# Kernel optimization log

Hardware: AMD Instinct MI355X
Metric: run time of the kernel (lower is better)

## Reference

```python
import jax, jax.numpy as jnp
import numpy as np

OBS = 256      # observation_space_size == state_vector_len
SV = 2047      # STATE_VECTORS = WMG_MAX_OBS
D = 256        # tfm_vec_size = 8 heads * 32 head_size
H = 8
HD = 32
L = 2          # TFM_NUM_LAYERS
FF = 1024      # TFM_HIDDEN_SIZE
ACH = 512      # AC_HIDDEN_LAYER_SIZE
A = 16         # action_space_size


def setup_inputs() -> dict:
    key = jax.random.key(0)
    ks = jax.random.split(key, 24)
    r = lambda k, s: (jax.random.normal(k, s, jnp.float32) * 0.02)
    inp = {
        "observation": jax.random.normal(ks[0], (OBS,), jnp.float32),
        "old_vectors": jax.random.normal(ks[1], (SV, OBS), jnp.float32),
        "W_core": r(ks[2], (OBS, D)), "b_core": jnp.zeros((D,), jnp.float32),
        # memo embedding takes cat(state_vec, age_onehot) of size OBS+SV
        "W_memo": r(ks[3], (OBS + SV, D)), "b_memo": jnp.zeros((D,), jnp.float32),
        "Wq": r(ks[4], (L, D, D)), "bq": jnp.zeros((L, D), jnp.float32),
        "Wk": r(ks[5], (L, D, D)), "bk": jnp.zeros((L, D), jnp.float32),
        "Wv": r(ks[6], (L, D, D)), "bv": jnp.zeros((L, D), jnp.float32),
        "Wo": r(ks[7], (L, D, D)), "bo": jnp.zeros((L, D), jnp.float32),
        "ln1_g": jnp.ones((L, D), jnp.float32), "ln1_b": jnp.zeros((L, D), jnp.float32),
        "ln2_g": jnp.ones((L, D), jnp.float32), "ln2_b": jnp.zeros((L, D), jnp.float32),
        "W_ff1": r(ks[8], (L, D, FF)), "b_ff1": jnp.zeros((L, FF), jnp.float32),
        "W_ff2": r(ks[9], (L, FF, D)), "b_ff2": jnp.zeros((L, D), jnp.float32),
        "aW1": r(ks[10], (D, ACH)), "ab1": jnp.zeros((ACH,), jnp.float32),
        "aW2": r(ks[11], (ACH, ACH)), "ab2": jnp.zeros((ACH,), jnp.float32),
        "aWo": r(ks[12], (ACH, A)), "abo": jnp.zeros((A,), jnp.float32),
        "cW1": r(ks[13], (D, ACH)), "cb1": jnp.zeros((ACH,), jnp.float32),
        "cW2": r(ks[14], (ACH, ACH)), "cb2": jnp.zeros((ACH,), jnp.float32),
        "cWo": r(ks[15], (ACH, 1)), "cbo": jnp.zeros((1,), jnp.float32),
    }
    return inp


def _ln(x, g, b, eps=1e-5):
    m = jnp.mean(x, axis=-1, keepdims=True)
    v = jnp.mean(jnp.square(x - m), axis=-1, keepdims=True)
    return (x - m) * jax.lax.rsqrt(v + eps) * g + b


def reference(observation, old_vectors, W_core, b_core, W_memo, b_memo,
              Wq, bq, Wk, bk, Wv, bv, Wo, bo,
              ln1_g, ln1_b, ln2_g, ln2_b, W_ff1, b_ff1, W_ff2, b_ff2,
              aW1, ab1, aW2, ab2, aWo, abo, cW1, cb1, cW2, cb2, cWo, cbo):
    # core embedding [D]
    emb0 = observation @ W_core + b_core
    # fused memo + age-onehot embedding: cat(vec_i, e_i) @ W_memo == vec_i @ W_memo[:OBS] + W_memo[OBS+i]
    memo_emb = old_vectors @ W_memo[:OBS] + W_memo[OBS:] + b_memo  # [SV, D]
    x = jnp.concatenate([emb0[None, :], memo_emb], axis=0)[None]   # [1, 1+SV, D]
    S = 1 + SV
    scale = 1.0 / np.sqrt(HD).astype(np.float32)
    for l in range(L):
        q = (x @ Wq[l] + bq[l]).reshape(1, S, H, HD)
        k = (x @ Wk[l] + bk[l]).reshape(1, S, H, HD)
        v = (x @ Wv[l] + bv[l]).reshape(1, S, H, HD)
        scores = jnp.einsum('bqhd,bkhd->bhqk', q, k) * scale       # [1,H,S,S]
        probs = jax.nn.softmax(scores, axis=-1)
        ctx = jnp.einsum('bhqk,bkhd->bqhd', probs, v).reshape(1, S, D)
        x = _ln(x + ctx @ Wo[l] + bo[l], ln1_g[l], ln1_b[l])
        h = jax.nn.gelu(x @ W_ff1[l] + b_ff1[l])
        x = _ln(x + h @ W_ff2[l] + b_ff2[l], ln2_g[l], ln2_b[l])
    t = x[:, 0, :]                                                 # [1, D]
    ha = jnp.tanh(jnp.tanh(t @ aW1 + ab1) @ aW2 + ab2)
    policy = ha @ aWo + abo                                        # [1, A] logits
    hc = jnp.tanh(jnp.tanh(t @ cW1 + cb1) @ cW2 + cb2)
    value_est = hc @ cWo + cbo                                     # [1, 1]
    # WMG_MAX_MEMOS == 0 path: new state vector is tanh(observation)
    new_vector = jnp.tanh(observation)                             # [OBS]
    return value_est, policy, new_vector
```

## Files before the change

kernel.cpp:

```cpp
#include <hip/hip_runtime.h>
#include <stdint.h>

typedef __attribute__((ext_vector_type(8))) short bf16x8;
typedef __attribute__((ext_vector_type(4))) float f32x4;

constexpr int kSEQ = 2048;
constexpr int kD   = 256;
constexpr int kHD  = 32;
constexpr int kFF  = 1024;
constexpr int kACH = 512;
constexpr int kA   = 16;

__device__ __forceinline__ unsigned short f2b(float f) {
  union { float f; unsigned int u; } v; v.f = f;
  unsigned int r = v.u + 0x7FFFu + ((v.u >> 16) & 1u);
  return (unsigned short)(r >> 16);
}

struct ConvTable {
  const float* src[14];
  int K[14];
  int N[14];
  int dst[14];
  int tstart[15];
};

union SharedU {
  struct { unsigned short lt[64][72]; } cv;
  struct { unsigned short Al[64][40]; unsigned short Bl[64][40]; } g64;
  struct { unsigned short Kl[64][40]; unsigned short Vt[32][72];
           unsigned short Pl[4][16][72]; } at;
  struct { unsigned short As[16][264]; float2 red[4][16]; } lg;
  struct { float tl[512]; float red[4][64]; } hd;
  struct { float ha[512]; float hc[512]; float vred[4]; } h3;
};

struct MegaParams {
  ConvTable tab;
  const float *obs, *oldv, *Wcore, *bcore, *bmemo, *Wmemo2;
  const float *bq, *bk, *bv, *bo, *ln1g, *ln1b, *ln2g, *ln2b, *bff1, *bff2;
  const float *aW1, *ab1, *aW2, *ab2, *aWo, *abo;
  const float *cW1, *cb1, *cW2, *cb2, *cWo, *cbo;
  float* xf; unsigned short* xb;
  unsigned short *qb, *kb, *vb, *hb, *wT;
  float *pacc, *pml, *h1, *h2, *out;
  int oMemo, oQKV[2], oWoT[2], oFF1[2], oFF2[2];
  int convJobs, nsplit, tpb;
};

__device__ void ph_conv(const MegaParams& p, SharedU& sh) {
  const int tid = threadIdx.x;
  for (int job = blockIdx.x; job <= p.convJobs; job += gridDim.x) {
    __syncthreads();
    if (job == p.convJobs) {
      float a = p.bcore[tid];
      #pragma unroll 8
      for (int k = 0; k < 256; k++) a += p.obs[k] * p.Wcore[k * kD + tid];
      p.xf[tid] = a;
      p.xb[tid] = f2b(a);
      continue;
    }
    int m = 0;
    while (job >= p.tab.tstart[m + 1]) m++;
    const int tloc = job - p.tab.tstart[m];
    const int N = p.tab.N[m], K = p.tab.K[m];
    const int ntile = N >> 6;
    const int k0 = (tloc / ntile) * 64, n0 = (tloc % ntile) * 64;
    const float* src = p.tab.src[m];
    {
      const int r = tid >> 2, c16 = (tid & 3) * 16;
      const float* sp = src + (size_t)(k0 + r) * N + n0 + c16;
      #pragma unroll
      for (int j = 0; j < 16; j++) sh.cv.lt[r][c16 + j] = f2b(sp[j]);
    }
    __syncthreads();
    {
      const int n = tid >> 2, kc = (tid & 3) * 16;
      unsigned short* dp = p.wT + p.tab.dst[m] + (size_t)(n0 + n) * K + k0 + kc;
      unsigned short g[16];
      #pragma unroll
      for (int j = 0; j < 16; j++) g[j] = sh.cv.lt[kc + j][n];
      *(bf16x8*)dp = *(bf16x8*)&g[0];
      *(bf16x8*)(dp + 8) = *(bf16x8*)&g[8];
    }
  }
}

template <int EPI, bool AF32>
__device__ __forceinline__ void gemm64_job(
    SharedU& sh, int m0, int n0, const void* Ap, int lda, int M, int K,
    const unsigned short* BT, const float* p0, const float* p1,
    const float* p2, void* o0, void* o1, void* o2) {
  const int tid = threadIdx.x;
  const int w = tid >> 6, l = tid & 63, lg = l >> 4, lr = l & 15;
  const int sr = tid >> 2, sk = (tid & 3) * 8;
  f32x4 acc[4];
  #pragma unroll
  for (int c = 0; c < 4; c++)
    #pragma unroll
    for (int i = 0; i < 4; i++) acc[c][i] = 0.f;

  auto loadA = [&](int k0) -> bf16x8 {
    bf16x8 av;
    if (m0 + sr < M) {
      if constexpr (AF32) {
        const float* ap = (const float*)Ap + (size_t)(m0 + sr) * lda + k0 + sk;
        #pragma unroll
        for (int j = 0; j < 8; j++) av[j] = (short)f2b(ap[j]);
      } else {
        av = *(const bf16x8*)((const unsigned short*)Ap +
                              (size_t)(m0 + sr) * lda + k0 + sk);
      }
    } else {
      #pragma unroll
      for (int j = 0; j < 8; j++) av[j] = 0;
    }
    return av;
  };

  bf16x8 av = loadA(0);
  bf16x8 bv = *(const bf16x8*)(BT + (size_t)(n0 + sr) * K + sk);

  for (int k0 = 0; k0 < K; k0 += 32) {
    __syncthreads();
    *(bf16x8*)&sh.g64.Al[sr][sk] = av;
    *(bf16x8*)&sh.g64.Bl[sr][sk] = bv;
    __syncthreads();
    if (k0 + 32 < K) {
      av = loadA(k0 + 32);
      bv = *(const bf16x8*)(BT + (size_t)(n0 + sr) * K + k0 + 32 + sk);
    }
    bf16x8 af = *(bf16x8*)&sh.g64.Al[w * 16 + lr][8 * lg];
    #pragma unroll
    for (int c = 0; c < 4; c++) {
      bf16x8 bf = *(bf16x8*)&sh.g64.Bl[c * 16 + lr][8 * lg];
      acc[c] = __builtin_amdgcn_mfma_f32_16x16x32_bf16(af, bf, acc[c], 0, 0, 0);
    }
  }

  #pragma unroll
  for (int c = 0; c < 4; c++) {
    #pragma unroll
    for (int i = 0; i < 4; i++) {
      const int gr = m0 + w * 16 + 4 * lg + i;
      const int gc = n0 + c * 16 + lr;
      if (gr >= M) continue;
      float v = acc[c][i];
      if constexpr (EPI == 0) {
        v += p0[gc] + p1[(size_t)gr * kD + gc];
        ((float*)o0)[(size_t)(gr + 1) * kD + gc] = v;
        ((unsigned short*)o1)[(size_t)(gr + 1) * kD + gc] = f2b(v);
      } else if constexpr (EPI == 1) {
        const int t = gc >> 8, cc = gc & 255;
        const float* bp = (t == 0) ? p0 : (t == 1 ? p1 : p2);
        unsigned short* op = (t == 0) ? (unsigned short*)o0
                              : (t == 1 ? (unsigned short*)o1
                                        : (unsigned short*)o2);
        v += bp[cc];
        if (t == 0) v *= 0.17677669529663687f;
        op[(size_t)gr * kD + cc] = f2b(v);
      } else {
        v += p0[gc];
        const float g =
            0.5f * v *
            (1.0f + tanhf(0.7978845608028654f * (v + 0.044715f * v * v * v)));
        ((unsigned short*)o0)[(size_t)gr * kFF + gc] = f2b(g);
      }
    }
  }
}

template <int EPI, bool AF32>
__device__ void ph_gemm(SharedU& sh, const void* Ap, int lda, int M, int K,
                        const unsigned short* BT, int Mtiles, int Ntiles,
                        const float* p0, const float* p1, const float* p2,
                        void* o0, void* o1, void* o2) {
  const int njobs = Mtiles * Ntiles;
  for (int job = blockIdx.x; job < njobs; job += gridDim.x) {
    const int m0 = (job % Mtiles) * 64, n0 = (job / Mtiles) * 64;
    gemm64_job<EPI, AF32>(sh, m0, n0, Ap, lda, M, K, BT, p0, p1, p2, o0, o1, o2);
  }
}

__device__ void attn_job(SharedU& sh, int qb_, int h, int s, int tpb,
                         const unsigned short* q, const unsigned short* k,
                         const unsigned short* v, float* pacc, float* pml) {
  const int tid = threadIdx.x;
  const int w = tid >> 6, l = tid & 63, lg = l >> 4, lr = l & 15;
  const int q0 = qb_ * 64;
  const int hoff = h * kHD;
  const int sr = tid >> 2, sk = (tid & 3) * 8;
  const int t0 = s * tpb;

  const bf16x8 qf =
      *(const bf16x8*)(q + (size_t)(q0 + w * 16 + lr) * kD + hoff + 8 * lg);

  float m_[4], l_[4];
  f32x4 acc[2];
  #pragma unroll
  for (int i = 0; i < 4; i++) { m_[i] = -1e30f; l_[i] = 0.f; }
  #pragma unroll
  for (int dt = 0; dt < 2; dt++)
    #pragma unroll
    for (int i = 0; i < 4; i++) acc[dt][i] = 0.f;

  bf16x8 kreg = *(const bf16x8*)(k + (size_t)(t0 * 64 + sr) * kD + hoff + sk);
  bf16x8 vreg = *(const bf16x8*)(v + (size_t)(t0 * 64 + sr) * kD + hoff + sk);

  for (int t = 0; t < tpb; t++) {
    __syncthreads();
    *(bf16x8*)&sh.at.Kl[sr][sk] = kreg;
    #pragma unroll
    for (int j = 0; j < 8; j++) sh.at.Vt[sk + j][sr] = (unsigned short)vreg[j];
    __syncthreads();
    if (t + 1 < tpb) {
      const size_t nx = (size_t)((t0 + t + 1) * 64 + sr) * kD + hoff + sk;
      kreg = *(const bf16x8*)(k + nx);
      vreg = *(const bf16x8*)(v + nx);
    }
    f32x4 sc[4];
    #pragma unroll
    for (int c = 0; c < 4; c++) {
      f32x4 z;
      #pragma unroll
      for (int i = 0; i < 4; i++) z[i] = 0.f;
      bf16x8 kf = *(bf16x8*)&sh.at.Kl[c * 16 + lr][8 * lg];
      sc[c] = __builtin_amdgcn_mfma_f32_16x16x32_bf16(qf, kf, z, 0, 0, 0);
    }
    float tm[4];
    #pragma unroll
    for (int i = 0; i < 4; i++)
      tm[i] = fmaxf(fmaxf(sc[0][i], sc[1][i]), fmaxf(sc[2][i], sc[3][i]));
    #pragma unroll
    for (int mm = 1; mm <= 8; mm <<= 1)
      #pragma unroll
      for (int i = 0; i < 4; i++) tm[i] = fmaxf(tm[i], __shfl_xor(tm[i], mm));
    float pv[4][4], rs[4], corr[4];
    #pragma unroll
    for (int i = 0; i < 4; i++) {
      const float nm = fmaxf(m_[i], tm[i]);
      corr[i] = __expf(m_[i] - nm);
      m_[i] = nm;
      rs[i] = 0.f;
    }
    #pragma unroll
    for (int c = 0; c < 4; c++)
      #pragma unroll
      for (int i = 0; i < 4; i++) {
        pv[c][i] = __expf(sc[c][i] - m_[i]);
        rs[i] += pv[c][i];
      }
    #pragma unroll
    for (int mm = 1; mm <= 8; mm <<= 1)
      #pragma unroll
      for (int i = 0; i < 4; i++) rs[i] += __shfl_xor(rs[i], mm);
    #pragma unroll
    for (int i = 0; i < 4; i++) {
      l_[i] = l_[i] * corr[i] + rs[i];
      acc[0][i] *= corr[i];
      acc[1][i] *= corr[i];
    }
    #pragma unroll
    for (int c = 0; c < 4; c++)
      #pragma unroll
      for (int i = 0; i < 4; i++)
        sh.at.Pl[w][4 * lg + i][c * 16 + lr] = f2b(pv[c][i]);
    __syncthreads();
    #pragma unroll
    for (int k2 = 0; k2 < 2; k2++) {
      bf16x8 pf = *(bf16x8*)&sh.at.Pl[w][lr][k2 * 32 + 8 * lg];
      #pragma unroll
      for (int dt = 0; dt < 2; dt++) {
        bf16x8 vf = *(bf16x8*)&sh.at.Vt[dt * 16 + lr][k2 * 32 + 8 * lg];
        acc[dt] = __builtin_amdgcn_mfma_f32_16x16x32_bf16(pf, vf, acc[dt], 0, 0, 0);
      }
    }
  }

  const int pb = s * 8 + h;
  float* pa = pacc + (size_t)pb * kSEQ * kHD;
  float* pm = pml + (size_t)pb * kSEQ * 2;
  #pragma unroll
  for (int dt = 0; dt < 2; dt++)
    #pragma unroll
    for (int i = 0; i < 4; i++) {
      const int gr = q0 + w * 16 + 4 * lg + i;
      pa[(size_t)gr * kHD + dt * 16 + lr] = acc[dt][i];
    }
  if (lr == 0) {
    #pragma unroll
    for (int i = 0; i < 4; i++) {
      const int gr = q0 + w * 16 + 4 * lg + i;
      float2 ml; ml.x = m_[i]; ml.y = l_[i];
      *(float2*)&pm[(size_t)gr * 2] = ml;
    }
  }
}

__device__ void ph_attn(const MegaParams& p, SharedU& sh) {
  const int njobs = 256 * p.nsplit;
  for (int job = blockIdx.x; job < njobs; job += gridDim.x) {
    const int qb_ = job & 31, h = (job >> 5) & 7, s = job >> 8;
    attn_job(sh, qb_, h, s, p.tpb, p.qb, p.kb, p.vb, p.pacc, p.pml);
  }
}

__device__ __forceinline__ void ln_write(SharedU& sh, float vloc[4][4], int r0,
                                         const float* gam, const float* bet,
                                         float* xf, unsigned short* xb) {
  const int tid = threadIdx.x;
  const int w = tid >> 6, l = tid & 63, lg = l >> 4, lr = l & 15;
  float ps[4], ps2[4];
  #pragma unroll
  for (int i = 0; i < 4; i++) {
    ps[i] = 0.f; ps2[i] = 0.f;
    #pragma unroll
    for (int c = 0; c < 4; c++) {
      ps[i] += vloc[c][i];
      ps2[i] += vloc[c][i] * vloc[c][i];
    }
  }
  #pragma unroll
  for (int mm = 1; mm <= 8; mm <<= 1)
    #pragma unroll
    for (int i = 0; i < 4; i++) {
      ps[i] += __shfl_xor(ps[i], mm);
      ps2[i] += __shfl_xor(ps2[i], mm);
    }
  if (lr == 0) {
    #pragma unroll
    for (int i = 0; i < 4; i++) {
      float2 t; t.x = ps[i]; t.y = ps2[i];
      sh.lg.red[w][4 * lg + i] = t;
    }
  }
  __syncthreads();
  #pragma unroll
  for (int i = 0; i < 4; i++) {
    const int ri = 4 * lg + i;
    float sx = 0.f, sx2 = 0.f;
    #pragma unroll
    for (int ww = 0; ww < 4; ww++) {
      float2 t = sh.lg.red[ww][ri];
      sx += t.x; sx2 += t.y;
    }
    const float mean = sx * (1.0f / 256.0f);
    const float var = sx2 * (1.0f / 256.0f) - mean * mean;
    const float rstd = rsqrtf(var + 1e-5f);
    const int gr = r0 + ri;
    #pragma unroll
    for (int c = 0; c < 4; c++) {
      const int col = w * 64 + c * 16 + lr;
      const float y = (vloc[c][i] - mean) * rstd * gam[col] + bet[col];
      xf[(size_t)gr * kD + col] = y;
      xb[(size_t)gr * kD + col] = f2b(y);
    }
  }
}

__device__ void ph_woln(const MegaParams& p, SharedU& sh, int lyr) {
  const unsigned short* BT = p.wT + p.oWoT[lyr];
  const float* bias = p.bo + lyr * kD;
  const float* gam = p.ln1g + lyr * kD;
  const float* bet = p.ln1b + lyr * kD;
  const int tid = threadIdx.x;
  const int w = tid >> 6, l = tid & 63, lg = l >> 4, lr = l & 15;
  for (int job = blockIdx.x; job < 128; job += gridDim.x) {
    const int r0 = job * 16;
    __syncthreads();
    {
      const int row = r0 + (tid >> 4);
      const int kc = (tid & 15) * 16;
      const int h_ = kc >> 5;
      float mx = -1e30f;
      float mlm[4], mll[4];
      for (int s2 = 0; s2 < p.nsplit; s2++) {
        const float2 t =
            *(const float2*)&p.pml[((size_t)(s2 * 8 + h_) * kSEQ + row) * 2];
        mlm[s2] = t.x; mll[s2] = t.y;
        mx = fmaxf(mx, t.x);
      }
      float L = 0.f, e[4];
      for (int s2 = 0; s2 < p.nsplit; s2++) {
        e[s2] = __expf(mlm[s2] - mx);
        L += mll[s2] * e[s2];
      }
      const float inv = 1.0f / L;
      const int d0 = kc & 31;
      float o[16];
      #pragma unroll
      for (int j = 0; j < 16; j++) o[j] = 0.f;
      for (int s2 = 0; s2 < p.nsplit; s2++) {
        const float* pa =
            p.pacc + ((size_t)(s2 * 8 + h_) * kSEQ + row) * kHD + d0;
        const float es = e[s2];
        #pragma unroll
        for (int j = 0; j < 16; j++) o[j] += pa[j] * es;
      }
      unsigned short* dst = &sh.lg.As[tid >> 4][kc];
      #pragma unroll
      for (int j = 0; j < 16; j++) dst[j] = f2b(o[j] * inv);
    }
    __syncthreads();
    f32x4 acc[4];
    #pragma unroll
    for (int c = 0; c < 4; c++)
      #pragma unroll
      for (int i = 0; i < 4; i++) acc[c][i] = 0.f;
    #pragma unroll 2
    for (int k0 = 0; k0 < 256; k0 += 32) {
      bf16x8 af = *(bf16x8*)&sh.lg.As[lr][k0 + 8 * lg];
      #pragma unroll
      for (int c = 0; c < 4; c++) {
        bf16x8 bf = *(const bf16x8*)(BT + (size_t)(w * 64 + c * 16 + lr) * 256 +
                                     k0 + 8 * lg);
        acc[c] = __builtin_amdgcn_mfma_f32_16x16x32_bf16(af, bf, acc[c], 0, 0, 0);
      }
    }
    float vloc[4][4];
    #pragma unroll
    for (int c = 0; c < 4; c++)
      #pragma unroll
      for (int i = 0; i < 4; i++) {
        const int col = w * 64 + c * 16 + lr;
        const int gr = r0 + 4 * lg + i;
        vloc[c][i] = acc[c][i] + bias[col] + p.xf[(size_t)gr * kD + col];
      }
    ln_write(sh, vloc, r0, gam, bet, p.xf, p.xb);
  }
}

__device__ void ph_ff2ln(const MegaParams& p, SharedU& sh, int lyr) {
  const unsigned short* BT = p.wT + p.oFF2[lyr];
  const float* bias = p.bff2 + lyr * kD;
  const float* gam = p.ln2g + lyr * kD;
  const float* bet = p.ln2b + lyr * kD;
  const int tid = threadIdx.x;
  const int w = tid >> 6, l = tid & 63, lg = l >> 4, lr = l & 15;
  for (int job = blockIdx.x; job < 128; job += gridDim.x) {
    const int r0 = job * 16;
    f32x4 acc[4];
    #pragma unroll
    for (int c = 0; c < 4; c++)
      #pragma unroll
      for (int i = 0; i < 4; i++) acc[c][i] = 0.f;
    const int srow = tid >> 4, skc = (tid & 15) * 16;
    const unsigned short* src = p.hb + (size_t)(r0 + srow) * kFF + skc;
    bf16x8 a0 = *(const bf16x8*)src;
    bf16x8 a1 = *(const bf16x8*)(src + 8);
    for (int kc = 0; kc < 1024; kc += 256) {
      __syncthreads();
      *(bf16x8*)&sh.lg.As[srow][skc] = a0;
      *(bf16x8*)&sh.lg.As[srow][skc + 8] = a1;
      __syncthreads();
      if (kc + 256 < 1024) {
        a0 = *(const bf16x8*)(src + kc + 256);
        a1 = *(const bf16x8*)(src + kc + 256 + 8);
      }
      #pragma unroll 2
      for (int k0 = 0; k0 < 256; k0 += 32) {
        bf16x8 af = *(bf16x8*)&sh.lg.As[lr][k0 + 8 * lg];
        #pragma unroll
        for (int c = 0; c < 4; c++) {
          bf16x8 bf = *(const bf16x8*)(
              BT + (size_t)(w * 64 + c * 16 + lr) * 1024 + kc + k0 + 8 * lg);
          acc[c] = __builtin_amdgcn_mfma_f32_16x16x32_bf16(af, bf, acc[c], 0, 0, 0);
        }
      }
    }
    float vloc[4][4];
    #pragma unroll
    for (int c = 0; c < 4; c++)
      #pragma unroll
      for (int i = 0; i < 4; i++) {
        const int col = w * 64 + c * 16 + lr;
        const int gr = r0 + 4 * lg + i;
        vloc[c][i] = acc[c][i] + bias[col] + p.xf[(size_t)gr * kD + col];
      }
    ln_write(sh, vloc, r0, gam, bet, p.xf, p.xb);
  }
}

__device__ void ph_h1(const MegaParams& p, SharedU& sh) {
  const int tid = threadIdx.x;
  for (int job = blockIdx.x; job < 16; job += gridDim.x) {
    __syncthreads();
    sh.hd.tl[tid] = p.xf[tid];
    __syncthreads();
    const int jj = job * 64;
    const bool actor = jj < 512;
    const float* W = actor ? p.aW1 : p.cW1;
    const float* b = actor ? p.ab1 : p.cb1;
    const int j0 = actor ? jj : jj - 512;
    const int ks = tid >> 6, j = tid & 63;
    float s = 0.f;
    #pragma unroll 4
    for (int k2 = ks * 64; k2 < ks * 64 + 64; k2++)
      s += sh.hd.tl[k2] * W[(size_t)k2 * kACH + j0 + j];
    sh.hd.red[ks][j] = s;
    __syncthreads();
    if (tid < 64) {
      float t = sh.hd.red[0][tid] + sh.hd.red[1][tid] + sh.hd.red[2][tid] +
                sh.hd.red[3][tid] + b[j0 + tid];
      p.h1[jj + tid] = tanhf(t);
    }
  }
}

__device__ void ph_h2(const MegaParams& p, SharedU& sh) {
  const int tid = threadIdx.x;
  for (int job = blockIdx.x; job < 16; job += gridDim.x) {
    __syncthreads();
    const int jj = job * 64;
    const bool actor = jj < 512;
    const float* hin = actor ? p.h1 : p.h1 + 512;
    sh.hd.tl[tid] = hin[tid];
    sh.hd.tl[tid + 256] = hin[tid + 256];
    __syncthreads();
    const float* W = actor ? p.aW2 : p.cW2;
    const float* b = actor ? p.ab2 : p.cb2;
    const int j0 = actor ? jj : jj - 512;
    const int ks = tid >> 6, j = tid & 63;
    float s = 0.f;
    #pragma unroll 4
    for (int k2 = ks * 128; k2 < ks * 128 + 128; k2++)
      s += sh.hd.tl[k2] * W[(size_t)k2 * kACH + j0 + j];
    sh.hd.red[ks][j] = s;
    __syncthreads();
    if (tid < 64) {
      float t = sh.hd.red[0][tid] + sh.hd.red[1][tid] + sh.hd.red[2][tid] +
                sh.hd.red[3][tid] + b[j0 + tid];
      p.h2[jj + tid] = tanhf(t);
    }
  }
}

__device__ void ph_h3(const MegaParams& p, SharedU& sh) {
  const int tid = threadIdx.x;
  for (int job = blockIdx.x; job < 1; job += gridDim.x) {
    __syncthreads();
    sh.h3.ha[tid] = p.h2[tid];
    sh.h3.ha[tid + 256] = p.h2[tid + 256];
    sh.h3.hc[tid] = p.h2[512 + tid];
    sh.h3.hc[tid + 256] = p.h2[768 + tid];
    __syncthreads();
    const int g = tid >> 4, lane16 = tid & 15;
    float s = 0.f;
    for (int k2 = lane16 * 32; k2 < lane16 * 32 + 32; k2++)
      s += sh.h3.ha[k2] * p.aWo[(size_t)k2 * kA + g];
    #pragma unroll
    for (int mm = 1; mm <= 8; mm <<= 1) s += __shfl_xor(s, mm);
    if (lane16 == 0) p.out[1 + g] = s + p.abo[g];
    float vv = sh.h3.hc[tid] * p.cWo[tid] + sh.h3.hc[tid + 256] * p.cWo[tid + 256];
    #pragma unroll
    for (int mm = 1; mm <= 32; mm <<= 1) vv += __shfl_xor(vv, mm);
    if ((tid & 63) == 0) sh.h3.vred[tid >> 6] = vv;
    __syncthreads();
    if (tid == 0)
      p.out[0] = sh.h3.vred[0] + sh.h3.vred[1] + sh.h3.vred[2] + sh.h3.vred[3] +
                 p.cbo[0];
    p.out[17 + tid] = tanhf(p.obs[tid]);
  }
}

__global__ __launch_bounds__(256) void k_conv(MegaParams p) { __shared__ SharedU sh; ph_conv(p, sh); }
__global__ __launch_bounds__(256) void k_memo(MegaParams p) {
  __shared__ SharedU sh;
  ph_gemm<0, true>(sh, p.oldv, 256, 2047, 256, p.wT + p.oMemo, 32, 4,
                   p.bmemo, p.Wmemo2, nullptr, p.xf, p.xb, nullptr);
}
__global__ __launch_bounds__(256) void k_qkv(MegaParams p, int lyr) {
  __shared__ SharedU sh;
  ph_gemm<1, false>(sh, p.xb, 256, 2048, 256, p.wT + p.oQKV[lyr], 32, 12,
                    p.bq + lyr * 256, p.bk + lyr * 256, p.bv + lyr * 256,
                    p.qb, p.kb, p.vb);
}
__global__ __launch_bounds__(256) void k_attn(MegaParams p) { __shared__ SharedU sh; ph_attn(p, sh); }
__global__ __launch_bounds__(256) void k_woln(MegaParams p, int lyr) { __shared__ SharedU sh; ph_woln(p, sh, lyr); }
__global__ __launch_bounds__(256) void k_ff1(MegaParams p, int lyr) {
  __shared__ SharedU sh;
  ph_gemm<2, false>(sh, p.xb, 256, 2048, 256, p.wT + p.oFF1[lyr], 32, 16,
                    p.bff1 + lyr * 1024, nullptr, nullptr, p.hb, nullptr, nullptr);
}
__global__ __launch_bounds__(256) void k_ff2ln(MegaParams p, int lyr) { __shared__ SharedU sh; ph_ff2ln(p, sh, lyr); }
__global__ __launch_bounds__(256) void k_h1(MegaParams p) { __shared__ SharedU sh; ph_h1(p, sh); }
__global__ __launch_bounds__(256) void k_h2(MegaParams p) { __shared__ SharedU sh; ph_h2(p, sh); }
__global__ __launch_bounds__(256) void k_h3(MegaParams p) { __shared__ SharedU sh; ph_h3(p, sh); }

extern "C" void kernel_launch(void* const* d_in, const int* in_sizes, int n_in,
                              void* d_out, int out_size, void* d_ws, size_t ws_size,
                              hipStream_t stream) {
  const float* obs   = (const float*)d_in[0];
  const float* oldv  = (const float*)d_in[1];
  const float* Wcore = (const float*)d_in[2];
  const float* bcore = (const float*)d_in[3];
  const float* Wmemo = (const float*)d_in[4];
  const float* bmemo = (const float*)d_in[5];
  const float* Wq    = (const float*)d_in[6];
  const float* bq    = (const float*)d_in[7];
  const float* Wk    = (const float*)d_in[8];
  const float* bk    = (const float*)d_in[9];
  const float* Wv    = (const float*)d_in[10];
  const float* bv    = (const float*)d_in[11];
  const float* Wo    = (const float*)d_in[12];
  const float* bo    = (const float*)d_in[13];
  const float* ln1g  = (const float*)d_in[14];
  const float* ln1b  = (const float*)d_in[15];
  const float* ln2g  = (const float*)d_in[16];
  const float* ln2b  = (const float*)d_in[17];
  const float* Wff1  = (const float*)d_in[18];
  const float* bff1  = (const float*)d_in[19];
  const float* Wff2  = (const float*)d_in[20];
  const float* bff2  = (const float*)d_in[21];

  MegaParams P;
  P.obs = obs; P.oldv = oldv; P.Wcore = Wcore; P.bcore = bcore;
  P.bmemo = bmemo; P.Wmemo2 = Wmemo + 256 * 256;
  P.bq = bq; P.bk = bk; P.bv = bv; P.bo = bo;
  P.ln1g = ln1g; P.ln1b = ln1b; P.ln2g = ln2g; P.ln2b = ln2b;
  P.bff1 = bff1; P.bff2 = bff2;
  P.aW1 = (const float*)d_in[22]; P.ab1 = (const float*)d_in[23];
  P.aW2 = (const float*)d_in[24]; P.ab2 = (const float*)d_in[25];
  P.aWo = (const float*)d_in[26]; P.abo = (const float*)d_in[27];
  P.cW1 = (const float*)d_in[28]; P.cb1 = (const float*)d_in[29];
  P.cW2 = (const float*)d_in[30]; P.cb2 = (const float*)d_in[31];
  P.cWo = (const float*)d_in[32]; P.cbo = (const float*)d_in[33];

  char* ws = (char*)d_ws;
  P.xf = (float*)(ws + 0);
  P.xb = (unsigned short*)(ws + (2u << 20));
  P.qb = (unsigned short*)(ws + (3u << 20));
  P.kb = (unsigned short*)(ws + (4u << 20));
  P.vb = (unsigned short*)(ws + (5u << 20));
  P.hb = (unsigned short*)(ws + (6u << 20));
  P.h1 = (float*)(ws + (10u << 20));
  P.h2 = (float*)(ws + (10u << 20) + 8192);
  P.wT = (unsigned short*)(ws + (10u << 20) + 65536);
  P.out = (float*)d_out;

  int nsplit = 4;
  const size_t paccOff = (size_t)14u << 20;
  while (nsplit > 1 &&
         paccOff + (size_t)nsplit * 8 * kSEQ * (kHD + 2) * 4 > ws_size)
    nsplit >>= 1;
  P.pacc = (float*)(ws + paccOff);
  P.pml = (float*)(ws + paccOff + (size_t)nsplit * 8 * kSEQ * kHD * 4);
  P.nsplit = nsplit;
  P.tpb = 32 / nsplit;

  P.oMemo = 0;
  int cur = 65536;
  for (int l2 = 0; l2 < 2; l2++) {
    P.oQKV[l2] = cur; cur += 196608;
    P.oWoT[l2] = cur; cur += 65536;
    P.oFF1[l2] = cur; cur += 262144;
    P.oFF2[l2] = cur; cur += 262144;
  }

  int idx = 0, ts = 0;
  auto add = [&](const float* s, int K, int N, int dst) {
    P.tab.src[idx] = s; P.tab.K[idx] = K; P.tab.N[idx] = N;
    P.tab.dst[idx] = dst; P.tab.tstart[idx] = ts;
    ts += (K >> 6) * (N >> 6); idx++;
  };
  add(Wmemo, 256, 256, P.oMemo);
  for (int l2 = 0; l2 < 2; l2++) {
    add(Wq + l2 * 65536, 256, 256, P.oQKV[l2]);
    add(Wk + l2 * 65536, 256, 256, P.oQKV[l2] + 65536);
    add(Wv + l2 * 65536, 256, 256, P.oQKV[l2] + 131072);
    add(Wo + l2 * 65536, 256, 256, P.oWoT[l2]);
    add(Wff1 + l2 * 262144, 256, 1024, P.oFF1[l2]);
    add(Wff2 + l2 * 262144, 1024, 256, P.oFF2[l2]);
  }
  P.tab.tstart[idx] = ts;
  P.convJobs = ts;

  k_conv<<<ts + 1, 256, 0, stream>>>(P);
  k_memo<<<128, 256, 0, stream>>>(P);
  for (int lyr = 0; lyr < 2; lyr++) {
    k_qkv<<<384, 256, 0, stream>>>(P, lyr);
    k_attn<<<256 * nsplit, 256, 0, stream>>>(P);
    k_woln<<<128, 256, 0, stream>>>(P, lyr);
    k_ff1<<<512, 256, 0, stream>>>(P, lyr);
    k_ff2ln<<<128, 256, 0, stream>>>(P, lyr);
  }
  k_h1<<<16, 256, 0, stream>>>(P);
  k_h2<<<16, 256, 0, stream>>>(P);
  k_h3<<<1, 256, 0, stream>>>(P);
}
```

Before: 234.2 us.

## Split FF2 into split-K partial GEMM plus LN reduce, shrink GEMM N-tiles

GEMM tiles narrow from 64x64 to 64x32 and grids double, giving more blocks on the memo, QKV and FF1 GEMMs. The fused FF2+LayerNorm kernel, which had only 128 blocks, becomes a split-K GEMM over four K chunks that writes fp32 partials. A separate row-wise kernel then sums the partials with bias and residual and applies LayerNorm. Attention splits rise from 4 to 8, with a simplified merge loop. The aim is better CU occupancy, at the cost of extra partial-sum traffic, one more launch per layer and less data reuse per tile.

```diff
diff --git a/kernel.cpp b/kernel.cpp
--- a/kernel.cpp
+++ b/kernel.cpp
@@ -27,7 +27,7 @@
 
 union SharedU {
   struct { unsigned short lt[64][72]; } cv;
-  struct { unsigned short Al[64][40]; unsigned short Bl[64][40]; } g64;
+  struct { unsigned short Al[64][40]; unsigned short Bl[32][40]; } g64;
   struct { unsigned short Kl[64][40]; unsigned short Vt[32][72];
            unsigned short Pl[4][16][72]; } at;
   struct { unsigned short As[16][264]; float2 red[4][16]; } lg;
@@ -43,7 +43,7 @@
   const float *cW1, *cb1, *cW2, *cb2, *cWo, *cbo;
   float* xf; unsigned short* xb;
   unsigned short *qb, *kb, *vb, *hb, *wT;
-  float *pacc, *pml, *h1, *h2, *out;
+  float *pacc, *pml, *pf, *h1, *h2, *out;
   int oMemo, oQKV[2], oWoT[2], oFF1[2], oFF2[2];
   int convJobs, nsplit, tpb;
 };
@@ -87,16 +87,17 @@
 }
 
 template <int EPI, bool AF32>
-__device__ __forceinline__ void gemm64_job(
-    SharedU& sh, int m0, int n0, const void* Ap, int lda, int M, int K,
-    const unsigned short* BT, const float* p0, const float* p1,
-    const float* p2, void* o0, void* o1, void* o2) {
+__device__ __forceinline__ void gemm_job(
+    SharedU& sh, int m0, int n0, const void* Ap, int lda, int M, int Kloop,
+    const unsigned short* BT, int ldb,
+    const float* p0, const float* p1, const float* p2,
+    void* o0, void* o1, void* o2) {
   const int tid = threadIdx.x;
   const int w = tid >> 6, l = tid & 63, lg = l >> 4, lr = l & 15;
   const int sr = tid >> 2, sk = (tid & 3) * 8;
-  f32x4 acc[4];
-  #pragma unroll
-  for (int c = 0; c < 4; c++)
+  f32x4 acc[2];
+  #pragma unroll
+  for (int c = 0; c < 2; c++)
     #pragma unroll
     for (int i = 0; i < 4; i++) acc[c][i] = 0.f;
 
@@ -119,27 +120,29 @@
   };
 
   bf16x8 av = loadA(0);
-  bf16x8 bv = *(const bf16x8*)(BT + (size_t)(n0 + sr) * K + sk);
-
-  for (int k0 = 0; k0 < K; k0 += 32) {
+  bf16x8 bv;
+  if (tid < 128) bv = *(const bf16x8*)(BT + (size_t)(n0 + sr) * ldb + sk);
+
+  for (int k0 = 0; k0 < Kloop; k0 += 32) {
     __syncthreads();
     *(bf16x8*)&sh.g64.Al[sr][sk] = av;
-    *(bf16x8*)&sh.g64.Bl[sr][sk] = bv;
-    __syncthreads();
-    if (k0 + 32 < K) {
+    if (tid < 128) *(bf16x8*)&sh.g64.Bl[sr][sk] = bv;
+    __syncthreads();
+    if (k0 + 32 < Kloop) {
       av = loadA(k0 + 32);
-      bv = *(const bf16x8*)(BT + (size_t)(n0 + sr) * K + k0 + 32 + sk);
+      if (tid < 128)
+        bv = *(const bf16x8*)(BT + (size_t)(n0 + sr) * ldb + k0 + 32 + sk);
     }
     bf16x8 af = *(bf16x8*)&sh.g64.Al[w * 16 + lr][8 * lg];
     #pragma unroll
-    for (int c = 0; c < 4; c++) {
+    for (int c = 0; c < 2; c++) {
       bf16x8 bf = *(bf16x8*)&sh.g64.Bl[c * 16 + lr][8 * lg];
       acc[c] = __builtin_amdgcn_mfma_f32_16x16x32_bf16(af, bf, acc[c], 0, 0, 0);
     }
   }
 
   #pragma unroll
-  for (int c = 0; c < 4; c++) {
+  for (int c = 0; c < 2; c++) {
     #pragma unroll
     for (int i = 0; i < 4; i++) {
       const int gr = m0 + w * 16 + 4 * lg + i;
@@ -159,12 +162,14 @@
         v += bp[cc];
         if (t == 0) v *= 0.17677669529663687f;
         op[(size_t)gr * kD + cc] = f2b(v);
-      } else {
+      } else if constexpr (EPI == 2) {
         v += p0[gc];
         const float g =
             0.5f * v *
             (1.0f + tanhf(0.7978845608028654f * (v + 0.044715f * v * v * v)));
         ((unsigned short*)o0)[(size_t)gr * kFF + gc] = f2b(g);
+      } else {
+        ((float*)o0)[(size_t)gr * kD + gc] = v;
       }
     }
   }
@@ -177,8 +182,21 @@
                         void* o0, void* o1, void* o2) {
   const int njobs = Mtiles * Ntiles;
   for (int job = blockIdx.x; job < njobs; job += gridDim.x) {
-    const int m0 = (job % Mtiles) * 64, n0 = (job / Mtiles) * 64;
-    gemm64_job<EPI, AF32>(sh, m0, n0, Ap, lda, M, K, BT, p0, p1, p2, o0, o1, o2);
+    const int m0 = (job % Mtiles) * 64, n0 = (job / Mtiles) * 32;
+    gemm_job<EPI, AF32>(sh, m0, n0, Ap, lda, M, K, BT, K, p0, p1, p2,
+                        o0, o1, o2);
+  }
+}
+
+__device__ void ph_ff2p(const MegaParams& p, SharedU& sh, int lyr) {
+  for (int job = blockIdx.x; job < 1024; job += gridDim.x) {
+    const int m0 = (job & 31) * 64;
+    const int n0 = ((job >> 5) & 7) * 32;
+    const int kc = (job >> 8) * 256;
+    gemm_job<3, false>(sh, m0, n0, p.hb + kc, kFF, 2048, 256,
+                       p.wT + p.oFF2[lyr] + kc, kFF,
+                       nullptr, nullptr, nullptr,
+                       p.pf + (size_t)(job >> 8) * kSEQ * kD, nullptr, nullptr);
   }
 }
 
@@ -268,11 +286,11 @@
     __syncthreads();
     #pragma unroll
     for (int k2 = 0; k2 < 2; k2++) {
-      bf16x8 pf = *(bf16x8*)&sh.at.Pl[w][lr][k2 * 32 + 8 * lg];
+      bf16x8 pf_ = *(bf16x8*)&sh.at.Pl[w][lr][k2 * 32 + 8 * lg];
       #pragma unroll
       for (int dt = 0; dt < 2; dt++) {
         bf16x8 vf = *(bf16x8*)&sh.at.Vt[dt * 16 + lr][k2 * 32 + 8 * lg];
-        acc[dt] = __builtin_amdgcn_mfma_f32_16x16x32_bf16(pf, vf, acc[dt], 0, 0, 0);
+        acc[dt] = __builtin_amdgcn_mfma_f32_16x16x32_bf16(pf_, vf, acc[dt], 0, 0, 0);
       }
     }
   }
@@ -373,30 +391,23 @@
       const int kc = (tid & 15) * 16;
       const int h_ = kc >> 5;
       float mx = -1e30f;
-      float mlm[4], mll[4];
-      for (int s2 = 0; s2 < p.nsplit; s2++) {
-        const float2 t =
-            *(const float2*)&p.pml[((size_t)(s2 * 8 + h_) * kSEQ + row) * 2];
-        mlm[s2] = t.x; mll[s2] = t.y;
-        mx = fmaxf(mx, t.x);
-      }
-      float L = 0.f, e[4];
-      for (int s2 = 0; s2 < p.nsplit; s2++) {
-        e[s2] = __expf(mlm[s2] - mx);
-        L += mll[s2] * e[s2];
-      }
-      const float inv = 1.0f / L;
+      for (int s2 = 0; s2 < p.nsplit; s2++)
+        mx = fmaxf(mx, p.pml[((size_t)(s2 * 8 + h_) * kSEQ + row) * 2]);
+      float L = 0.f;
       const int d0 = kc & 31;
       float o[16];
       #pragma unroll
       for (int j = 0; j < 16; j++) o[j] = 0.f;
       for (int s2 = 0; s2 < p.nsplit; s2++) {
-        const float* pa =
-            p.pacc + ((size_t)(s2 * 8 + h_) * kSEQ + row) * kHD + d0;
-        const float es = e[s2];
+        const size_t pb = (size_t)(s2 * 8 + h_) * kSEQ + row;
+        const float2 t = *(const float2*)&p.pml[pb * 2];
+        const float es = __expf(t.x - mx);
+        L += t.y * es;
+        const float* pa = p.pacc + pb * kHD + d0;
         #pragma unroll
         for (int j = 0; j < 16; j++) o[j] += pa[j] * es;
       }
+      const float inv = 1.0f / L;
       unsigned short* dst = &sh.lg.As[tid >> 4][kc];
       #pragma unroll
       for (int j = 0; j < 16; j++) dst[j] = f2b(o[j] * inv);
@@ -430,55 +441,44 @@
   }
 }
 
-__device__ void ph_ff2ln(const MegaParams& p, SharedU& sh, int lyr) {
-  const unsigned short* BT = p.wT + p.oFF2[lyr];
+__device__ void ph_ln2r(const MegaParams& p, int lyr) {
   const float* bias = p.bff2 + lyr * kD;
   const float* gam = p.ln2g + lyr * kD;
   const float* bet = p.ln2b + lyr * kD;
-  const int tid = threadIdx.x;
-  const int w = tid >> 6, l = tid & 63, lg = l >> 4, lr = l & 15;
-  for (int job = blockIdx.x; job < 128; job += gridDim.x) {
-    const int r0 = job * 16;
-    f32x4 acc[4];
-    #pragma unroll
-    for (int c = 0; c < 4; c++)
-      #pragma unroll
-      for (int i = 0; i < 4; i++) acc[c][i] = 0.f;
-    const int srow = tid >> 4, skc = (tid & 15) * 16;
-    const unsigned short* src = p.hb + (size_t)(r0 + srow) * kFF + skc;
-    bf16x8 a0 = *(const bf16x8*)src;
-    bf16x8 a1 = *(const bf16x8*)(src + 8);
-    for (int kc = 0; kc < 1024; kc += 256) {
-      __syncthreads();
-      *(bf16x8*)&sh.lg.As[srow][skc] = a0;
-      *(bf16x8*)&sh.lg.As[srow][skc + 8] = a1;
-      __syncthreads();
-      if (kc + 256 < 1024) {
-        a0 = *(const bf16x8*)(src + kc + 256);
-        a1 = *(const bf16x8*)(src + kc + 256 + 8);
-      }
-      #pragma unroll 2
-      for (int k0 = 0; k0 < 256; k0 += 32) {
-        bf16x8 af = *(bf16x8*)&sh.lg.As[lr][k0 + 8 * lg];
-        #pragma unroll
-        for (int c = 0; c < 4; c++) {
-          bf16x8 bf = *(const bf16x8*)(
-              BT + (size_t)(w * 64 + c * 16 + lr) * 1024 + kc + k0 + 8 * lg);
-          acc[c] = __builtin_amdgcn_mfma_f32_16x16x32_bf16(af, bf, acc[c], 0, 0, 0);
-        }
-      }
-    }
-    float vloc[4][4];
-    #pragma unroll
-    for (int c = 0; c < 4; c++)
-      #pragma unroll
-      for (int i = 0; i < 4; i++) {
-        const int col = w * 64 + c * 16 + lr;
-        const int gr = r0 + 4 * lg + i;
-        vloc[c][i] = acc[c][i] + bias[col] + p.xf[(size_t)gr * kD + col];
-      }
-    ln_write(sh, vloc, r0, gam, bet, p.xf, p.xb);
-  }
+  const int w = threadIdx.x >> 6, l = threadIdx.x & 63;
+  const int row = blockIdx.x * 4 + w;
+  f32x4 v = *(const f32x4*)(p.xf + (size_t)row * kD + l * 4);
+  f32x4 b4 = *(const f32x4*)(bias + l * 4);
+  #pragma unroll
+  for (int i = 0; i < 4; i++) v[i] += b4[i];
+  #pragma unroll
+  for (int s = 0; s < 4; s++) {
+    f32x4 t = *(const f32x4*)(p.pf + ((size_t)s * kSEQ + row) * kD + l * 4);
+    #pragma unroll
+    for (int i = 0; i < 4; i++) v[i] += t[i];
+  }
+  float su = v[0] + v[1] + v[2] + v[3];
+  #pragma unroll
+  for (int mm = 1; mm < 64; mm <<= 1) su += __shfl_xor(su, mm);
+  const float mn = su * (1.0f / 256.0f);
+  const float d0 = v[0] - mn, d1 = v[1] - mn, d2 = v[2] - mn, d3 = v[3] - mn;
+  float s2 = d0 * d0 + d1 * d1 + d2 * d2 + d3 * d3;
+  #pragma unroll
+  for (int mm = 1; mm < 64; mm <<= 1) s2 += __shfl_xor(s2, mm);
+  const float rstd = rsqrtf(s2 * (1.0f / 256.0f) + 1e-5f);
+  f32x4 g4 = *(const f32x4*)(gam + l * 4);
+  f32x4 be4 = *(const f32x4*)(bet + l * 4);
+  f32x4 y;
+  y[0] = d0 * rstd * g4[0] + be4[0];
+  y[1] = d1 * rstd * g4[1] + be4[1];
+  y[2] = d2 * rstd * g4[2] + be4[2];
+  y[3] = d3 * rstd * g4[3] + be4[3];
+  *(f32x4*)(p.xf + (size_t)row * kD + l * 4) = y;
+  unsigned long long pk = (unsigned long long)f2b(y[0]) |
+                          ((unsigned long long)f2b(y[1]) << 16) |
+                          ((unsigned long long)f2b(y[2]) << 32) |
+                          ((unsigned long long)f2b(y[3]) << 48);
+  *(unsigned long long*)(p.xb + (size_t)row * kD + l * 4) = pk;
 }
 
 __device__ void ph_h1(const MegaParams& p, SharedU& sh) {
@@ -566,12 +566,12 @@
 __global__ __launch_bounds__(256) void k_conv(MegaParams p) { __shared__ SharedU sh; ph_conv(p, sh); }
 __global__ __launch_bounds__(256) void k_memo(MegaParams p) {
   __shared__ SharedU sh;
-  ph_gemm<0, true>(sh, p.oldv, 256, 2047, 256, p.wT + p.oMemo, 32, 4,
+  ph_gemm<0, true>(sh, p.oldv, 256, 2047, 256, p.wT + p.oMemo, 32, 8,
                    p.bmemo, p.Wmemo2, nullptr, p.xf, p.xb, nullptr);
 }
 __global__ __launch_bounds__(256) void k_qkv(MegaParams p, int lyr) {
   __shared__ SharedU sh;
-  ph_gemm<1, false>(sh, p.xb, 256, 2048, 256, p.wT + p.oQKV[lyr], 32, 12,
+  ph_gemm<1, false>(sh, p.xb, 256, 2048, 256, p.wT + p.oQKV[lyr], 32, 24,
                     p.bq + lyr * 256, p.bk + lyr * 256, p.bv + lyr * 256,
                     p.qb, p.kb, p.vb);
 }
@@ -579,10 +579,11 @@
 __global__ __launch_bounds__(256) void k_woln(MegaParams p, int lyr) { __shared__ SharedU sh; ph_woln(p, sh, lyr); }
 __global__ __launch_bounds__(256) void k_ff1(MegaParams p, int lyr) {
   __shared__ SharedU sh;
-  ph_gemm<2, false>(sh, p.xb, 256, 2048, 256, p.wT + p.oFF1[lyr], 32, 16,
+  ph_gemm<2, false>(sh, p.xb, 256, 2048, 256, p.wT + p.oFF1[lyr], 32, 32,
                     p.bff1 + lyr * 1024, nullptr, nullptr, p.hb, nullptr, nullptr);
 }
-__global__ __launch_bounds__(256) void k_ff2ln(MegaParams p, int lyr) { __shared__ SharedU sh; ph_ff2ln(p, sh, lyr); }
+__global__ __launch_bounds__(256) void k_ff2p(MegaParams p, int lyr) { __shared__ SharedU sh; ph_ff2p(p, sh, lyr); }
+__global__ __launch_bounds__(256) void k_ln2r(MegaParams p, int lyr) { ph_ln2r(p, lyr); }
 __global__ __launch_bounds__(256) void k_h1(MegaParams p) { __shared__ SharedU sh; ph_h1(p, sh); }
 __global__ __launch_bounds__(256) void k_h2(MegaParams p) { __shared__ SharedU sh; ph_h2(p, sh); }
 __global__ __launch_bounds__(256) void k_h3(MegaParams p) { __shared__ SharedU sh; ph_h3(p, sh); }
@@ -638,13 +639,17 @@
   P.wT = (unsigned short*)(ws + (10u << 20) + 65536);
   P.out = (float*)d_out;
 
-  int nsplit = 4;
+  int nsplit = 8;
   const size_t paccOff = (size_t)14u << 20;
+  const size_t pmlOff  = (size_t)31u << 20;
+  const size_t pfOff   = (size_t)33u << 20;
   while (nsplit > 1 &&
-         paccOff + (size_t)nsplit * 8 * kSEQ * (kHD + 2) * 4 > ws_size)
+         (paccOff + (size_t)nsplit * 8 * kSEQ * kHD * 4 > pmlOff ||
+          pfOff + (size_t)4 * kSEQ * kD * 4 > ws_size))
     nsplit >>= 1;
   P.pacc = (float*)(ws + paccOff);
-  P.pml = (float*)(ws + paccOff + (size_t)nsplit * 8 * kSEQ * kHD * 4);
+  P.pml  = (float*)(ws + pmlOff);
+  P.pf   = (float*)(ws + pfOff);
   P.nsplit = nsplit;
   P.tpb = 32 / nsplit;
 
@@ -676,13 +681,14 @@
   P.convJobs = ts;
 
   k_conv<<<ts + 1, 256, 0, stream>>>(P);
-  k_memo<<<128, 256, 0, stream>>>(P);
+  k_memo<<<256, 256, 0, stream>>>(P);
   for (int lyr = 0; lyr < 2; lyr++) {
-    k_qkv<<<384, 256, 0, stream>>>(P, lyr);
+    k_qkv<<<768, 256, 0, stream>>>(P, lyr);
     k_attn<<<256 * nsplit, 256, 0, stream>>>(P);
     k_woln<<<128, 256, 0, stream>>>(P, lyr);
-    k_ff1<<<512, 256, 0, stream>>>(P, lyr);
-    k_ff2ln<<<128, 256, 0, stream>>>(P, lyr);
+    k_ff1<<<1024, 256, 0, stream>>>(P, lyr);
+    k_ff2p<<<1024, 256, 0, stream>>>(P, lyr);
+    k_ln2r<<<512, 256, 0, stream>>>(P, lyr);
   }
   k_h1<<<16, 256, 0, stream>>>(P);
   k_h2<<<16, 256, 0, stream>>>(P);
```

New measurement: 207.3 us. 1.13x faster.
